# Optimization experiments

Measured on AMD Instinct MI355X. Metric: run time of the kernel, lower is better.

## Reference

```python
import jax, jax.numpy as jnp
import numpy as np

B, N, D, H = 4, 1024, 1024, 16
HD = D // H  # 64
EPS = 1e-5


def rotate_half(t):
    # unflatten last dim to (..., HD//2, 2), swap-and-negate, flatten back
    t2 = t.reshape(t.shape[:-1] + (HD // 2, 2))
    x1, x2 = t2[..., 0], t2[..., 1]
    return jnp.stack((-x2, x1), axis=-1).reshape(t.shape)


def setup_inputs() -> dict:
    key = jax.random.key(0)
    ks = jax.random.split(key, 12)
    s = 0.02
    return {
        "x": jax.random.normal(ks[0], (B, N, D), jnp.float32),
        "encoding": jax.random.uniform(ks[1], (2, B, 1, N, HD), jnp.float32),
        "Wqkv_w": jax.random.normal(ks[2], (3 * D, D), jnp.float32) * s,
        "Wqkv_b": jnp.zeros((3 * D,), jnp.float32),
        "out_w": jax.random.normal(ks[3], (D, D), jnp.float32) * s,
        "out_b": jnp.zeros((D,), jnp.float32),
        "ffn1_w": jax.random.normal(ks[4], (2 * D, 2 * D), jnp.float32) * s,
        "ffn1_b": jnp.zeros((2 * D,), jnp.float32),
        "ln_g": jnp.ones((2 * D,), jnp.float32),
        "ln_b": jnp.zeros((2 * D,), jnp.float32),
        "ffn2_w": jax.random.normal(ks[5], (D, 2 * D), jnp.float32) * s,
        "ffn2_b": jnp.zeros((D,), jnp.float32),
    }


def reference(x, encoding, Wqkv_w, Wqkv_b, out_w, out_b,
              ffn1_w, ffn1_b, ln_g, ln_b, ffn2_w, ffn2_b):
    b, n, d = x.shape
    # fused QKV projection: [B,N,3D] -> [B,H,N,HD,3]
    qkv = x @ Wqkv_w.T + Wqkv_b
    qkv = qkv.reshape(b, n, H, HD, 3).transpose(0, 2, 1, 3, 4)
    q, k, v = qkv[..., 0], qkv[..., 1], qkv[..., 2]
    # cached rotary embedding: t*cos + rotate_half(t)*sin
    q = q * encoding[0] + rotate_half(q) * encoding[1]
    k = k * encoding[0] + rotate_half(k) * encoding[1]
    # scaled dot-product attention (mask is None in this path)
    scale = HD ** -0.5
    sim = jnp.einsum('bhid,bhjd->bhij', q, k) * scale
    attn = jax.nn.softmax(sim, axis=-1)
    ctx = jnp.einsum('bhij,bhjd->bhid', attn, v)
    ctx = ctx.transpose(0, 2, 1, 3).reshape(b, n, d)
    message = ctx @ out_w.T + out_b
    # FFN on concat([x, message]) with interposed LayerNorm + GELU (exact)
    h = jnp.concatenate([x, message], axis=-1) @ ffn1_w.T + ffn1_b
    mu = h.mean(-1, keepdims=True)
    var = ((h - mu) ** 2).mean(-1, keepdims=True)
    h = (h - mu) * jax.lax.rsqrt(var + EPS) * ln_g + ln_b
    h = jax.nn.gelu(h, approximate=False)
    return x + h @ ffn2_w.T + ffn2_b
```

## Files before the change

kernel.cpp:

```cpp
#include <hip/hip_runtime.h>
#include <hip/hip_bf16.h>
#include <math.h>

#define B_ 4
#define N_ 1024
#define D_ 1024
#define H_ 16
#define HD_ 64
#define M_ (B_*N_)

typedef __hip_bfloat16 bf16;
using floatx4 = __attribute__((ext_vector_type(4))) float;
using shortx8 = __attribute__((ext_vector_type(8))) short;

__device__ __forceinline__ float to_f(bf16 v) { return __bfloat162float(v); }
__device__ __forceinline__ float s2f(short v) {
    unsigned u = ((unsigned)(unsigned short)v) << 16;
    return __builtin_bit_cast(float, u);
}
__device__ __forceinline__ unsigned short bf_bits(float x) {
    bf16 h = __float2bfloat16(x);
    return *reinterpret_cast<unsigned short*>(&h);
}

#define GLOBAL_AS __attribute__((address_space(1)))
#define LDS_AS    __attribute__((address_space(3)))
__device__ __forceinline__ void load_lds16(const void* g, void* l) {
    __builtin_amdgcn_global_load_lds((const GLOBAL_AS unsigned int*)g,
                                     (LDS_AS unsigned int*)l, 16, 0, 0);
}

__device__ __forceinline__ void storec(float* p, float v) { *p = v; }
__device__ __forceinline__ void storec(bf16*  p, float v) { *p = __float2bfloat16(v); }

template<typename TC, bool RESID, bool SPLIT, int BM, int BN, int BK>
__global__ __launch_bounds__(256)
void mgemm(const bf16* __restrict__ A, int lda,
           const bf16* __restrict__ A2, int lda2, int K1,
           const bf16* __restrict__ W, int ldw,
           const float* __restrict__ bias,
           const float* __restrict__ resid, int ldr,
           TC* __restrict__ C, int ldc,
           int M, int N, int K)
{
    constexpr int MT  = BM / 32;
    constexpr int NT  = BN / 32;
    constexpr int KH  = BK / 32;
    constexpr int CH  = BK / 8;
    constexpr int ASZ = BM * BK;
    constexpr int BSZ = BN * BK;
    constexpr int APASS = (BM * CH) / 256;
    constexpr int BPASS = (BN * CH) / 256;
    __shared__ short lds[2 * (ASZ + BSZ)];

    int t = threadIdx.x;
    int lane = t & 63, quad = lane >> 4, l15 = lane & 15;
    int wave = t >> 6, wm = wave & 1, wn = wave >> 1;

    int gx = gridDim.x;
    int nwg = gx * gridDim.y;
    int p = blockIdx.y * gx + blockIdx.x;
    int bid;
    if (nwg & 7) bid = p;
    else         bid = (p & 7) * (nwg >> 3) + (p >> 3);
    int seg = bid / (8 * gx);
    int rem = bid - seg * 8 * gx;
    int bx = rem >> 3;
    int by = seg * 8 + (rem & 7);
    int row0 = by * BM, col0 = bx * BN;

    const short* Ag  = (const short*)A;
    const short* A2g = (const short*)A2;
    const short* Wg  = (const short*)W;

    auto swz = [](int r, int c) -> int {
        if constexpr (CH == 4) return c ^ ((r >> 1) & 3);
        else                   return c ^ (r & 7);
    };

    auto stage = [&](int buf, int k0) {
        short* As = lds + buf * (ASZ + BSZ);
        short* Bs = As + ASZ;
        #pragma unroll
        for (int pass = 0; pass < APASS; ++pass) {
            int idx = pass * 256 + t;
            int r = idx / CH, c = idx % CH;
            int cs = swz(r, c) << 3;
            int wub = (pass * 256 + (t & 192)) * 8;
            const short* asrc;
            if (SPLIT && k0 >= K1)
                asrc = A2g + (size_t)(row0 + r) * lda2 + (k0 - K1) + cs;
            else
                asrc = Ag + (size_t)(row0 + r) * lda + k0 + cs;
            load_lds16(asrc, &As[wub]);
        }
        #pragma unroll
        for (int pass = 0; pass < BPASS; ++pass) {
            int idx = pass * 256 + t;
            int r = idx / CH, c = idx % CH;
            int cs = swz(r, c) << 3;
            int wub = (pass * 256 + (t & 192)) * 8;
            load_lds16(Wg + (size_t)(col0 + r) * ldw + k0 + cs, &Bs[wub]);
        }
    };

    floatx4 acc[MT][NT];
    #pragma unroll
    for (int mt = 0; mt < MT; ++mt)
        #pragma unroll
        for (int nt = 0; nt < NT; ++nt)
            acc[mt][nt] = (floatx4){0.f, 0.f, 0.f, 0.f};

    stage(0, 0);
    int buf = 0;
    for (int k0 = 0; k0 < K; k0 += BK, buf ^= 1) {
        __syncthreads();

        if (k0 + BK < K) stage(buf ^ 1, k0 + BK);

        const short* As = lds + buf * (ASZ + BSZ);
        const short* Bs = As + ASZ;
        shortx8 af[MT][KH], bfv[NT][KH];
        #pragma unroll
        for (int mt = 0; mt < MT; ++mt) {
            int ar = wm * (BM / 2) + mt * 16 + l15;
            #pragma unroll
            for (int kk = 0; kk < KH; ++kk)
                af[mt][kk] = *(const shortx8*)&As[ar * BK + (swz(ar, kk * 4 + quad) << 3)];
        }
        #pragma unroll
        for (int nt = 0; nt < NT; ++nt) {
            int br = wn * (BN / 2) + nt * 16 + l15;
            #pragma unroll
            for (int kk = 0; kk < KH; ++kk)
                bfv[nt][kk] = *(const shortx8*)&Bs[br * BK + (swz(br, kk * 4 + quad) << 3)];
        }
        #pragma unroll
        for (int kk = 0; kk < KH; ++kk)
            #pragma unroll
            for (int mt = 0; mt < MT; ++mt)
                #pragma unroll
                for (int nt = 0; nt < NT; ++nt)
                    acc[mt][nt] = __builtin_amdgcn_mfma_f32_16x16x32_bf16(
                        af[mt][kk], bfv[nt][kk], acc[mt][nt], 0, 0, 0);
    }

    #pragma unroll
    for (int mt = 0; mt < MT; ++mt) {
        #pragma unroll
        for (int nt = 0; nt < NT; ++nt) {
            int col = col0 + wn * (BN / 2) + nt * 16 + l15;
            float bv = bias[col];
            #pragma unroll
            for (int r = 0; r < 4; ++r) {
                int row = row0 + wm * (BM / 2) + mt * 16 + quad * 4 + r;
                float v = acc[mt][nt][r] + bv;
                if (RESID) v += resid[(size_t)row * ldr + col];
                storec(&C[(size_t)row * ldc + col], v);
            }
        }
    }
}

__global__ void f2b_all(const float* __restrict__ s0, bf16* __restrict__ d0,
                        const float* __restrict__ s1, bf16* __restrict__ d1,
                        const float* __restrict__ s2, bf16* __restrict__ d2,
                        const float* __restrict__ s3, bf16* __restrict__ d3,
                        const float* __restrict__ s4, bf16* __restrict__ d4)
{
    int blk = blockIdx.x;
    const float* s; bf16* d; int base;
    if      (blk < 4096)  { s = s0; d = d0; base = blk; }
    else if (blk < 7168)  { s = s1; d = d1; base = blk - 4096; }
    else if (blk < 8192)  { s = s2; d = d2; base = blk - 7168; }
    else if (blk < 12288) { s = s3; d = d3; base = blk - 8192; }
    else                  { s = s4; d = d4; base = blk - 12288; }
    int i = base * 1024 + threadIdx.x * 4;
    float4 v = *(const float4*)&s[i];
    d[i + 0] = __float2bfloat16(v.x);
    d[i + 1] = __float2bfloat16(v.y);
    d[i + 2] = __float2bfloat16(v.z);
    d[i + 3] = __float2bfloat16(v.w);
}

#define RS 196
__global__ __launch_bounds__(256)
void rope_all(const bf16* __restrict__ qkv, const float* __restrict__ enc,
              bf16* __restrict__ q, bf16* __restrict__ k, bf16* __restrict__ vt)
{
    __shared__ short raw[64 * RS];
    int n0 = blockIdx.x * 64, h = blockIdx.y, b = blockIdx.z;
    int t = threadIdx.x;
    const short* qg = (const short*)qkv;

    {
        int row = t >> 2, off = (t & 3) * 48;
        const short* src = qg + ((size_t)(b * N_ + n0 + row)) * 3072 + h * 192 + off;
        uint4 u[3];
        u[0] = ((const uint4*)src)[0];
        u[1] = ((const uint4*)src)[1];
        u[2] = ((const uint4*)src)[2];
        uint4 u2[3];
        u2[0] = ((const uint4*)src)[3];
        u2[1] = ((const uint4*)src)[4];
        u2[2] = ((const uint4*)src)[5];
        uint2* dst = (uint2*)&raw[row * RS + off];
        const uint2* p = (const uint2*)u;
        #pragma unroll
        for (int i = 0; i < 6; ++i) dst[i] = p[i];
        const uint2* p2 = (const uint2*)u2;
        #pragma unroll
        for (int i = 0; i < 6; ++i) dst[6 + i] = p2[i];
    }
    __syncthreads();

    size_t bh = (size_t)(b * H_ + h);
    {
        int d = t & 63, g0 = t >> 6;
        int dp = d ^ 1;
        float sgn = (d & 1) ? 1.0f : -1.0f;
        #pragma unroll
        for (int i = 0; i < 16; ++i) {
            int nl = g0 + 4 * i;
            const short* r = &raw[nl * RS];
            float qv = s2f(r[3 * d]),  kv = s2f(r[3 * d + 1]);
            float qp = s2f(r[3 * dp]), kp = s2f(r[3 * dp + 1]);
            size_t ei = ((size_t)(b * N_ + n0 + nl)) * HD_ + d;
            float c = enc[ei];
            float s = enc[(size_t)B_ * N_ * HD_ + ei];
            size_t o = (bh * N_ + n0 + nl) * HD_ + d;
            q[o] = __float2bfloat16(qv * c + sgn * qp * s);
            k[o] = __float2bfloat16(kv * c + sgn * kp * s);
        }
    }
    {
        int nl = t & 63, g0 = t >> 6;
        #pragma unroll
        for (int i = 0; i < 16; ++i) {
            int dt = g0 + 4 * i;
            vt[(bh * HD_ + dt) * N_ + n0 + nl] =
                *reinterpret_cast<bf16*>(&raw[nl * RS + 3 * dt + 2]);
        }
    }
}

__global__ __launch_bounds__(256, 2)
void fattn(const bf16* __restrict__ q, const bf16* __restrict__ k,
           const bf16* __restrict__ vt, bf16* __restrict__ ctx)
{
    const int i0 = blockIdx.x * 128;
    const int h = blockIdx.y, b = blockIdx.z;
    const int t = threadIdx.x;
    const int lane = t & 63;
    const int w = t >> 6;
    const int quad = lane >> 4, l15 = lane & 15;

    __shared__ alignas(16) short Ks[2][64 * 72];
    __shared__ alignas(16) short Vs[2][64 * 72];
    __shared__ alignas(16) short Ps[128 * 72];

    const size_t bh = (size_t)(b * H_ + h) * N_;
    const size_t bhv = (size_t)(b * H_ + h) * HD_;
    const short* qg = (const short*)q;
    const short* kg = (const short*)k;
    const short* vg = (const short*)vt;

    shortx8 qf[2][2];
    #pragma unroll
    for (int rt = 0; rt < 2; ++rt) {
        const short* qrow = qg + (bh + i0 + w * 32 + rt * 16 + l15) * HD_;
        qf[rt][0] = *(const shortx8*)(qrow + quad * 8);
        qf[rt][1] = *(const shortx8*)(qrow + 32 + quad * 8);
    }

    floatx4 O[2][4];
    #pragma unroll
    for (int rt = 0; rt < 2; ++rt)
        #pragma unroll
        for (int dt = 0; dt < 4; ++dt) O[rt][dt] = (floatx4){0.f, 0.f, 0.f, 0.f};
    float lsum[2] = {0.f, 0.f};

    const int srow = t >> 2, soff = (t & 3) * 16;
    const short* kst = kg + (bh + srow) * HD_ + soff;
    const short* vst = vg + (bhv + srow) * N_ + soff;

    {
        uint4 a0 = ((const uint4*)kst)[0];
        uint4 a1 = ((const uint4*)kst)[1];
        uint4 b0 = ((const uint4*)vst)[0];
        uint4 b1 = ((const uint4*)vst)[1];
        *(uint4*)&Ks[0][srow * 72 + soff]     = a0;
        *(uint4*)&Ks[0][srow * 72 + soff + 8] = a1;
        *(uint4*)&Vs[0][srow * 72 + soff]     = b0;
        *(uint4*)&Vs[0][srow * 72 + soff + 8] = b1;
    }

    uint4 ka0, ka1, va0, va1;
    for (int it = 0; it < N_ / 64; ++it) {
        const int cur = it & 1;
        __syncthreads();

        if (it + 1 < N_ / 64) {
            const int j1 = (it + 1) * 64;
            const short* kn = kst + (size_t)j1 * HD_;
            const short* vn = vst + j1;
            ka0 = ((const uint4*)kn)[0];
            ka1 = ((const uint4*)kn)[1];
            va0 = ((const uint4*)vn)[0];
            va1 = ((const uint4*)vn)[1];
        }

        floatx4 ST[4][2];
        __builtin_amdgcn_s_setprio(1);
        #pragma unroll
        for (int kt = 0; kt < 4; ++kt) {
            shortx8 a0 = *(const shortx8*)&Ks[cur][(kt * 16 + l15) * 72 + quad * 8];
            shortx8 a1 = *(const shortx8*)&Ks[cur][(kt * 16 + l15) * 72 + 32 + quad * 8];
            #pragma unroll
            for (int rt = 0; rt < 2; ++rt) {
                floatx4 c = (floatx4){0.f, 0.f, 0.f, 0.f};
                c = __builtin_amdgcn_mfma_f32_16x16x32_bf16(a0, qf[rt][0], c, 0, 0, 0);
                c = __builtin_amdgcn_mfma_f32_16x16x32_bf16(a1, qf[rt][1], c, 0, 0, 0);
                ST[kt][rt] = c;
            }
        }
        __builtin_amdgcn_s_setprio(0);

        #pragma unroll
        for (int kt = 0; kt < 4; ++kt)
            #pragma unroll
            for (int rt = 0; rt < 2; ++rt) {
                unsigned short pk[4];
                #pragma unroll
                for (int r = 0; r < 4; ++r) {
                    float e = __expf(ST[kt][rt][r] * 0.125f);
                    lsum[rt] += e;
                    pk[r] = bf_bits(e);
                }
                *(uint2*)&Ps[(w * 32 + rt * 16 + l15) * 72 + kt * 16 + quad * 4] =
                    *(const uint2*)pk;
            }

        shortx8 pa[2][2];
        #pragma unroll
        for (int rt = 0; rt < 2; ++rt) {
            pa[rt][0] = *(const shortx8*)&Ps[(w * 32 + rt * 16 + l15) * 72 + quad * 8];
            pa[rt][1] = *(const shortx8*)&Ps[(w * 32 + rt * 16 + l15) * 72 + 32 + quad * 8];
        }
        __builtin_amdgcn_s_setprio(1);
        #pragma unroll
        for (int dt = 0; dt < 4; ++dt) {
            shortx8 vb0 = *(const shortx8*)&Vs[cur][(dt * 16 + l15) * 72 + quad * 8];
            shortx8 vb1 = *(const shortx8*)&Vs[cur][(dt * 16 + l15) * 72 + 32 + quad * 8];
            #pragma unroll
            for (int rt = 0; rt < 2; ++rt) {
                O[rt][dt] = __builtin_amdgcn_mfma_f32_16x16x32_bf16(pa[rt][0], vb0, O[rt][dt], 0, 0, 0);
                O[rt][dt] = __builtin_amdgcn_mfma_f32_16x16x32_bf16(pa[rt][1], vb1, O[rt][dt], 0, 0, 0);
            }
        }
        __builtin_amdgcn_s_setprio(0);

        if (it + 1 < N_ / 64) {
            *(uint4*)&Ks[cur ^ 1][srow * 72 + soff]     = ka0;
            *(uint4*)&Ks[cur ^ 1][srow * 72 + soff + 8] = ka1;
            *(uint4*)&Vs[cur ^ 1][srow * 72 + soff]     = va0;
            *(uint4*)&Vs[cur ^ 1][srow * 72 + soff + 8] = va1;
        }
    }

    #pragma unroll
    for (int rt = 0; rt < 2; ++rt) {
        float rs = lsum[rt];
        rs += __shfl_xor(rs, 16);
        rs += __shfl_xor(rs, 32);
        #pragma unroll
        for (int r = 0; r < 4; ++r) {
            float inv = 1.0f / __shfl(rs, quad * 4 + r);
            int row = i0 + w * 32 + rt * 16 + quad * 4 + r;
            #pragma unroll
            for (int dt = 0; dt < 4; ++dt)
                ctx[((size_t)(b * N_ + row)) * D_ + h * HD_ + dt * 16 + l15] =
                    __float2bfloat16(O[rt][dt][r] * inv);
        }
    }
}

__global__ void ln_gelu(bf16* __restrict__ hbuf, const float* __restrict__ g,
                        const float* __restrict__ beta)
{
    int row = blockIdx.x;
    int t = threadIdx.x;
    short* hr = (short*)hbuf + (size_t)row * 2048;

    shortx8 v = *(const shortx8*)&hr[t * 8];
    float vals[8];
    float s = 0.f, s2 = 0.f;
    #pragma unroll
    for (int l = 0; l < 8; ++l) {
        float x = s2f(v[l]);
        vals[l] = x; s += x; s2 += x * x;
    }
    #pragma unroll
    for (int off = 32; off >= 1; off >>= 1) {
        s  += __shfl_xor(s,  off);
        s2 += __shfl_xor(s2, off);
    }
    __shared__ float ws_[4], ws2_[4];
    if ((t & 63) == 0) { ws_[t >> 6] = s; ws2_[t >> 6] = s2; }
    __syncthreads();
    float S  = ws_[0] + ws_[1] + ws_[2] + ws_[3];
    float S2 = ws2_[0] + ws2_[1] + ws2_[2] + ws2_[3];

    float mu  = S * (1.0f / 2048.0f);
    float var = S2 * (1.0f / 2048.0f) - mu * mu;
    float rstd = rsqrtf(var + 1e-5f);

    float4 g0 = *(const float4*)&g[t * 8];
    float4 g1 = *(const float4*)&g[t * 8 + 4];
    float4 b0 = *(const float4*)&beta[t * 8];
    float4 b1 = *(const float4*)&beta[t * 8 + 4];
    float gv[8] = {g0.x, g0.y, g0.z, g0.w, g1.x, g1.y, g1.z, g1.w};
    float bv[8] = {b0.x, b0.y, b0.z, b0.w, b1.x, b1.y, b1.z, b1.w};

    shortx8 o;
    #pragma unroll
    for (int l = 0; l < 8; ++l) {
        float xn = (vals[l] - mu) * rstd * gv[l] + bv[l];
        float ge = 0.5f * xn * (1.0f + erff(xn * 0.70710678118654752f));
        o[l] = (short)bf_bits(ge);
    }
    *(shortx8*)&hr[t * 8] = o;
}

extern "C" void kernel_launch(void* const* d_in, const int* in_sizes, int n_in,
                              void* d_out, int out_size, void* d_ws, size_t ws_size,
                              hipStream_t stream)
{
    const float* x      = (const float*)d_in[0];
    const float* enc    = (const float*)d_in[1];
    const float* Wqkv_w = (const float*)d_in[2];
    const float* Wqkv_b = (const float*)d_in[3];
    const float* out_w  = (const float*)d_in[4];
    const float* out_b  = (const float*)d_in[5];
    const float* ffn1_w = (const float*)d_in[6];
    const float* ffn1_b = (const float*)d_in[7];
    const float* ln_g   = (const float*)d_in[8];
    const float* ln_b   = (const float*)d_in[9];
    const float* ffn2_w = (const float*)d_in[10];
    const float* ffn2_b = (const float*)d_in[11];
    float* out = (float*)d_out;

    float* ws = (float*)d_ws;
    bf16* qkv16 = (bf16*)ws;
    bf16* ctx16 = (bf16*)ws;
    bf16* h16   = (bf16*)(ws + 2097152);
    bf16* q16   = (bf16*)(ws + 6291456);
    bf16* k16   = q16 + 2097152;
    bf16* vt16  = k16 + 2097152;
    bf16* msg16 = (bf16*)(ws + 6291456);
    bf16* x16   = (bf16*)(ws + 12582912);
    bf16* wq16  = (bf16*)(ws + 14680064);
    bf16* wo16  = wq16 + 3145728;
    bf16* wf1   = wo16 + 1048576;
    bf16* wf2   = wf1 + 4194304;

    f2b_all<<<14336, 256, 0, stream>>>(x, x16, Wqkv_w, wq16, out_w, wo16,
                                       ffn1_w, wf1, ffn2_w, wf2);

    dim3 g1(3072 / 192, 4096 / 128);
    mgemm<bf16, false, false, 128, 192, 64><<<g1, 256, 0, stream>>>(
        x16, 1024, nullptr, 0, 0, wq16, 1024, Wqkv_b, nullptr, 0,
        qkv16, 3072, 4096, 3072, 1024);

    dim3 gr(16, 16, 4);
    rope_all<<<gr, 256, 0, stream>>>(qkv16, enc, q16, k16, vt16);

    dim3 ga(N_ / 128, H_, B_);
    fattn<<<ga, 256, 0, stream>>>(q16, k16, vt16, ctx16);

    dim3 g2(1024 / 64, 4096 / 128);
    mgemm<bf16, false, false, 128, 64, 64><<<g2, 256, 0, stream>>>(
        ctx16, 1024, nullptr, 0, 0, wo16, 1024, out_b, nullptr, 0,
        msg16, 1024, 4096, 1024, 1024);

    dim3 g3(2048 / 128, 4096 / 128);
    mgemm<bf16, false, true, 128, 128, 64><<<g3, 256, 0, stream>>>(
        x16, 1024, msg16, 1024, 1024, wf1, 2048, ffn1_b, nullptr, 0,
        h16, 2048, 4096, 2048, 2048);

    ln_gelu<<<4096, 256, 0, stream>>>(h16, ln_g, ln_b);

    dim3 g4(1024 / 64, 4096 / 128);
    mgemm<float, true, false, 128, 64, 64><<<g4, 256, 0, stream>>>(
        h16, 2048, nullptr, 0, 0, wf2, 2048, ffn2_b, x, 1024,
        out, 1024, 4096, 1024, 2048);
}
```

Before: 265.5 us.

## Software-pipeline QK^T of next tile with softmax-PV of current tile in attention

```diff
diff --git a/kernel.cpp b/kernel.cpp
--- a/kernel.cpp
+++ b/kernel.cpp
@@ -294,28 +294,24 @@
         *(uint4*)&Vs[0][srow * 72 + soff]     = b0;
         *(uint4*)&Vs[0][srow * 72 + soff + 8] = b1;
     }
+    __syncthreads();
 
     uint4 ka0, ka1, va0, va1;
-    for (int it = 0; it < N_ / 64; ++it) {
-        const int cur = it & 1;
-        __syncthreads();
-
-        if (it + 1 < N_ / 64) {
-            const int j1 = (it + 1) * 64;
-            const short* kn = kst + (size_t)j1 * HD_;
-            const short* vn = vst + j1;
-            ka0 = ((const uint4*)kn)[0];
-            ka1 = ((const uint4*)kn)[1];
-            va0 = ((const uint4*)vn)[0];
-            va1 = ((const uint4*)vn)[1];
-        }
-
-        floatx4 ST[4][2];
+    {
+        const short* kn = kst + (size_t)64 * HD_;
+        const short* vn = vst + 64;
+        ka0 = ((const uint4*)kn)[0];
+        ka1 = ((const uint4*)kn)[1];
+        va0 = ((const uint4*)vn)[0];
+        va1 = ((const uint4*)vn)[1];
+    }
+
+    auto qkt = [&](const short* Kbuf, floatx4 ST[4][2]) {
         __builtin_amdgcn_s_setprio(1);
         #pragma unroll
         for (int kt = 0; kt < 4; ++kt) {
-            shortx8 a0 = *(const shortx8*)&Ks[cur][(kt * 16 + l15) * 72 + quad * 8];
-            shortx8 a1 = *(const shortx8*)&Ks[cur][(kt * 16 + l15) * 72 + 32 + quad * 8];
+            shortx8 a0 = *(const shortx8*)&Kbuf[(kt * 16 + l15) * 72 + quad * 8];
+            shortx8 a1 = *(const shortx8*)&Kbuf[(kt * 16 + l15) * 72 + 32 + quad * 8];
             #pragma unroll
             for (int rt = 0; rt < 2; ++rt) {
                 floatx4 c = (floatx4){0.f, 0.f, 0.f, 0.f};
@@ -325,7 +321,9 @@
             }
         }
         __builtin_amdgcn_s_setprio(0);
-
+    };
+
+    auto exppv = [&](int cur, floatx4 ST[4][2]) {
         #pragma unroll
         for (int kt = 0; kt < 4; ++kt)
             #pragma unroll
@@ -340,7 +338,6 @@
                 *(uint2*)&Ps[(w * 32 + rt * 16 + l15) * 72 + kt * 16 + quad * 4] =
                     *(const uint2*)pk;
             }
-
         shortx8 pa[2][2];
         #pragma unroll
         for (int rt = 0; rt < 2; ++rt) {
@@ -359,14 +356,42 @@
             }
         }
         __builtin_amdgcn_s_setprio(0);
-
-        if (it + 1 < N_ / 64) {
-            *(uint4*)&Ks[cur ^ 1][srow * 72 + soff]     = ka0;
-            *(uint4*)&Ks[cur ^ 1][srow * 72 + soff + 8] = ka1;
-            *(uint4*)&Vs[cur ^ 1][srow * 72 + soff]     = va0;
-            *(uint4*)&Vs[cur ^ 1][srow * 72 + soff + 8] = va1;
-        }
-    }
+    };
+
+    floatx4 STp[4][2];
+    qkt(Ks[0], STp);
+
+    #pragma unroll 2
+    for (int it = 0; it < 15; ++it) {
+        const int nb = (it + 1) & 1;
+        __syncthreads();
+
+        *(uint4*)&Ks[nb][srow * 72 + soff]     = ka0;
+        *(uint4*)&Ks[nb][srow * 72 + soff + 8] = ka1;
+        *(uint4*)&Vs[nb][srow * 72 + soff]     = va0;
+        *(uint4*)&Vs[nb][srow * 72 + soff + 8] = va1;
+
+        if (it + 2 < 16) {
+            const short* kn = kst + (size_t)((it + 2) * 64) * HD_;
+            const short* vn = vst + (it + 2) * 64;
+            ka0 = ((const uint4*)kn)[0];
+            ka1 = ((const uint4*)kn)[1];
+            va0 = ((const uint4*)vn)[0];
+            va1 = ((const uint4*)vn)[1];
+        }
+        __syncthreads();
+
+        floatx4 STn[4][2];
+        qkt(Ks[nb], STn);
+        exppv(it & 1, STp);
+
+        #pragma unroll
+        for (int kt = 0; kt < 4; ++kt)
+            #pragma unroll
+            for (int rt = 0; rt < 2; ++rt)
+                STp[kt][rt] = STn[kt][rt];
+    }
+    exppv(1, STp);
 
     #pragma unroll
     for (int rt = 0; rt < 2; ++rt) {
```

Measured after the change: 432.7 us. +63.0%, slower.
